# Optimization experiments

Hardware: AMD Instinct MI355X
Metric: run time of the kernel (lower is better)

Reference implementation:

```python
import jax, jax.numpy as jnp
import numpy as np

ARRAY_SIZE = 128   # crossbar rows
CBITS = 4          # psum ADC bits
LEV = 2 ** (CBITS - 1)
ALPHA = ARRAY_SIZE / LEV   # psum quant step
EPS = 1e-5

# ---- binary activation / weight quant with STE (hardtanh grad) ----
@jax.custom_vjp
def ste_sign(x):
    return jnp.where(x >= 0, 1.0, -1.0).astype(x.dtype)

def _sign_fwd(x):
    return ste_sign(x), x

def _sign_bwd(x, g):
    return (g * (jnp.abs(x) <= 1.0).astype(g.dtype),)

ste_sign.defvjp(_sign_fwd, _sign_bwd)

# ---- psum (partial-sum) quantization: cbits-level ADC over each crossbar array ----
@jax.custom_vjp
def psum_quant(p):
    return jnp.clip(jnp.round(p / ALPHA), -LEV, LEV - 1) * ALPHA

def _pq_fwd(p):
    return psum_quant(p), p

def _pq_bwd(p, g):
    return (g * (jnp.abs(p) <= ARRAY_SIZE).astype(g.dtype),)

psum_quant.defvjp(_pq_fwd, _pq_bwd)

# ---- layers ----
def bn(x, p):
    g, b, m, v = p  # each [C]
    sh = (1, -1) + (1,) * (x.ndim - 2)
    return (x - m.reshape(sh)) * (g.reshape(sh) / jnp.sqrt(v.reshape(sh) + EPS)) + b.reshape(sh)

def maxpool2(x):
    return jax.lax.reduce_window(x, -jnp.inf, jax.lax.max, (1, 1, 2, 2), (1, 1, 2, 2), 'VALID')

def conv_same(x, w):
    return jax.lax.conv_general_dilated(x, w, (1, 1), 'SAME')

def psum_conv(x, w):
    # crossbar-mapped conv: input channels split into groups of arraySize//(kh*kw),
    # each group conv'd separately, psum-quantized (ADC), then accumulated.
    O, Cin, kh, kw = w.shape
    chunk = max(1, ARRAY_SIZE // (kh * kw))
    G = -(-Cin // chunk)
    pad = G * chunk - Cin
    xp = jnp.pad(x, ((0, 0), (0, pad), (0, 0), (0, 0)))
    wp = jnp.pad(w, ((0, 0), (0, pad), (0, 0), (0, 0)))
    B, _, H, W = x.shape
    xg = xp.reshape(B, G, chunk, H, W).transpose(1, 0, 2, 3, 4)   # [G,B,c,H,W]
    wg = wp.reshape(O, G, chunk, kh, kw).transpose(1, 0, 2, 3, 4)  # [G,O,c,kh,kw]
    ps = jax.vmap(conv_same)(xg, wg)                               # [G,B,O,H,W]
    return psum_quant(ps).sum(0)

def psum_linear(x, w):
    # x [B,D], w [O,D]; D divisible by ARRAY_SIZE
    B, D = x.shape
    O = w.shape[0]
    G = D // ARRAY_SIZE
    ps = jnp.einsum('bgc,ogc->gbo', x.reshape(B, G, ARRAY_SIZE), w.reshape(O, G, ARRAY_SIZE))
    return psum_quant(ps).sum(0)


def setup_inputs() -> dict:
    key = jax.random.key(0)
    ks = iter(jax.random.split(key, 64))
    def nrm(shape, s=0.05):
        return jax.random.normal(next(ks), shape, jnp.float32) * s
    def bnp(C):
        return jnp.stack([jax.random.uniform(next(ks), (C,), jnp.float32) + 0.5,
                          nrm((C,), 0.1), nrm((C,), 0.1),
                          jax.random.uniform(next(ks), (C,), jnp.float32) + 0.5])
    return dict(
        x=jax.random.normal(next(ks), (64, 3, 32, 32), jnp.float32),
        conv0_w=nrm((128, 3, 3, 3)), bn0=bnp(128),
        w1=nrm((128, 128, 3, 3)), bn1=bnp(128),
        w2=nrm((256, 128, 3, 3)), bn2=bnp(256),
        w3=nrm((256, 256, 3, 3)), bn3=bnp(256),
        w4=nrm((512, 256, 3, 3)), bn4=bnp(512),
        w5=nrm((512, 512, 3, 3)), bn5=bnp(512),
        fc1_w=nrm((1024, 8192)), bnf1=bnp(1024),
        fc2_w=nrm((1024, 1024)), bnf2=bnp(1024),
        out_w=nrm((10, 1024)), out_b=nrm((10,)), bnout=bnp(10),
    )


def reference(x, conv0_w, bn0, w1, bn1, w2, bn2, w3, bn3, w4, bn4, w5, bn5,
              fc1_w, bnf1, fc2_w, bnf2, out_w, out_b, bnout):
    h = conv_same(x, conv0_w)                       # full-precision first conv
    h = ste_sign(bn(h, bn0))
    h = psum_conv(h, ste_sign(w1)); h = maxpool2(h); h = ste_sign(bn(h, bn1))
    h = psum_conv(h, ste_sign(w2)); h = ste_sign(bn(h, bn2))
    h = psum_conv(h, ste_sign(w3)); h = maxpool2(h); h = ste_sign(bn(h, bn3))
    h = psum_conv(h, ste_sign(w4)); h = ste_sign(bn(h, bn4))
    h = psum_conv(h, ste_sign(w5)); h = maxpool2(h); h = ste_sign(bn(h, bn5))
    h = h.reshape(h.shape[0], -1)                   # [B, 8192]
    h = ste_sign(bn(psum_linear(h, ste_sign(fc1_w)), bnf1))
    h = bn(psum_linear(h, ste_sign(fc2_w)), bnf2)   # abits=32 -> identity nonlinear
    h = h @ out_w.T + out_b
    return bn(h, bnout)
```

## Files before the change

### kernel.cpp

```cpp
#include <hip/hip_runtime.h>
#include <cstdint>
#include <cstddef>

using bf16x8 = __attribute__((ext_vector_type(8))) short;
using f32x4  = __attribute__((ext_vector_type(4))) float;
using u32x4  = __attribute__((ext_vector_type(4))) unsigned int;

#define DI __device__ __forceinline__

DI float pq16(float ps) {
    float q = rintf(ps * 0.0625f);
    q = fminf(7.f, fmaxf(-8.f, q));
    return q * 16.f;
}

DI float bnv(float x, float g, float b, float m, float v) {
    return (x - m) * (g / sqrtf(v + 1e-5f)) + b;
}

DI unsigned short sgn_bf16(float v) {
    return (v >= 0.f) ? (unsigned short)0x3F80 : (unsigned short)0xBF80;
}

__global__ __launch_bounds__(256)
void k_conv0(const float* __restrict__ x, const float* __restrict__ w,
             const float* __restrict__ bnp, unsigned short* __restrict__ out) {
    __shared__ float sX[3][3][36];
    const int b = blockIdx.x >> 5, y = blockIdx.x & 31;
    const int tid = threadIdx.x;
    const int o = tid & 127, xc = tid >> 7;

    for (int i = tid; i < 3 * 3 * 36; i += 256) {
        int col = i % 36, rr = (i / 36) % 3, c = i / 108;
        int gy = y + rr - 1, gx = col - 1;
        float v = 0.f;
        if ((unsigned)gy < 32u && (unsigned)gx < 32u)
            v = x[((b * 3 + c) * 32 + gy) * 32 + gx];
        sX[c][rr][col] = v;
    }
    float wr[27];
    const float* wp = w + o * 27;
    #pragma unroll
    for (int t = 0; t < 27; ++t) wr[t] = wp[t];
    __syncthreads();

    const float bg = bnp[o], bb = bnp[128 + o], bm = bnp[256 + o], bv = bnp[384 + o];
    unsigned short* op = out + ((size_t)(b * 32 + y) * 32) * 128 + o;

    #pragma unroll
    for (int q = 0; q < 4; ++q) {
        float acc0 = 0.f, acc1 = 0.f, acc2 = 0.f, acc3 = 0.f;
        const int X0 = xc * 16 + q * 4;
        #pragma unroll
        for (int c = 0; c < 3; ++c)
            #pragma unroll
            for (int ky = 0; ky < 3; ++ky) {
                float xv0 = sX[c][ky][X0 + 0], xv1 = sX[c][ky][X0 + 1];
                float xv2 = sX[c][ky][X0 + 2], xv3 = sX[c][ky][X0 + 3];
                float xv4 = sX[c][ky][X0 + 4], xv5 = sX[c][ky][X0 + 5];
                float w0 = wr[c * 9 + ky * 3 + 0];
                float w1 = wr[c * 9 + ky * 3 + 1];
                float w2 = wr[c * 9 + ky * 3 + 2];
                acc0 += xv0 * w0 + xv1 * w1 + xv2 * w2;
                acc1 += xv1 * w0 + xv2 * w1 + xv3 * w2;
                acc2 += xv2 * w0 + xv3 * w1 + xv4 * w2;
                acc3 += xv3 * w0 + xv4 * w1 + xv5 * w2;
            }
        op[(size_t)(X0 + 0) * 128] = sgn_bf16(bnv(acc0, bg, bb, bm, bv));
        op[(size_t)(X0 + 1) * 128] = sgn_bf16(bnv(acc1, bg, bb, bm, bv));
        op[(size_t)(X0 + 2) * 128] = sgn_bf16(bnv(acc2, bg, bb, bm, bv));
        op[(size_t)(X0 + 3) * 128] = sgn_bf16(bnv(acc3, bg, bb, bm, bv));
    }
}

__global__ __launch_bounds__(256)
void k_pack_w(const float* __restrict__ w, unsigned short* __restrict__ wpk,
              int Cin, int O, int G) {
    int idx = blockIdx.x * 256 + threadIdx.x;
    int total = G * O * 160;
    if (idx >= total) return;
    int c = idx & 15;
    int tap = (idx >> 4) % 10;
    int rest = idx / 160;
    int o = rest % O, g = rest / O;
    unsigned short v = 0;
    int cg = g * 14 + c;
    if (tap < 9 && c < 14 && cg < Cin)
        v = sgn_bf16(w[((size_t)o * Cin + cg) * 9 + tap]);
    wpk[idx] = v;
}

template <int H, int W, int Cin, int O, int G, int RH, int RW, int POOLMODE>
__global__ __launch_bounds__(256)
void k_conv_mfma(const unsigned int* __restrict__ act,
                 const unsigned short* __restrict__ wpk,
                 const float* __restrict__ bnp,
                 unsigned short* __restrict__ outa,
                 unsigned short* __restrict__ a5p) {
    constexpr int SH = RH + 2, SW = RW + 2;
    constexpr int MS = RH * RW / 16;
    constexpr int NREGX = W / RW;
    static_assert(POOLMODE != 1 || RW == 16, "pool mode 1 needs RW=16");
    static_assert(POOLMODE != 2 || (RW == 8 && MS == 4), "pool mode 2 needs 8x8");

    __shared__ __align__(16) unsigned int sA[SH * SW * 12];

    const int tid  = threadIdx.x;
    const int regY = (int)blockIdx.x / NREGX, regX = (int)blockIdx.x % NREGX;
    const int o0   = blockIdx.y * 64;
    const int b    = blockIdx.z;

    const int lane = tid & 63, wv = tid >> 6;
    const int n  = lane & 15;
    const int kb = lane >> 4;
    const int hb = kb >> 1, ch = kb & 1;

    int baseA[MS];
    #pragma unroll
    for (int ms = 0; ms < MS; ++ms) {
        int p = ms * 16 + n;
        int y = p / RW, x = p % RW;
        baseA[ms] = (y * SW + x) * 48 + ch * 16;
    }

    float tot[MS][4];
    #pragma unroll
    for (int ms = 0; ms < MS; ++ms) {
        tot[ms][0] = 0.f; tot[ms][1] = 0.f; tot[ms][2] = 0.f; tot[ms][3] = 0.f;
    }

    const unsigned short* wrow = wpk + ((size_t)o0 + wv * 16 + n) * 160 + ch * 8;

    #pragma unroll 1
    for (int g = 0; g < G; ++g) {
        const int rem_dw = (Cin - g * 14) >> 1;
        for (int i = tid; i < SH * SW * 8; i += 256) {
            int cp = i & 7, slot = i >> 3;
            int yy = slot / SW, xx = slot - yy * SW;
            int gy = regY * RH + yy - 1, gx = regX * RW + xx - 1;
            unsigned int v = 0;
            if (cp < 7 && cp < rem_dw &&
                (unsigned)gy < (unsigned)H && (unsigned)gx < (unsigned)W)
                v = act[(((size_t)b * H + gy) * W + gx) * (Cin / 2) + g * 7 + cp];
            sA[slot * 12 + cp] = v;
        }
        const unsigned short* wg = wrow + (size_t)g * O * 160;
        bf16x8 bq[5];
        #pragma unroll
        for (int s = 0; s < 5; ++s) {
            int tap = 2 * s + hb;
            bq[s] = *(const bf16x8*)(wg + tap * 16);
        }
        __syncthreads();

        const char* sAc = (const char*)sA;
        #pragma unroll
        for (int ms = 0; ms < MS; ++ms) {
            f32x4 acc = {0.f, 0.f, 0.f, 0.f};
            #pragma unroll
            for (int s = 0; s < 5; ++s) {
                const int t0 = 2 * s, t1 = 2 * s + 1;
                const int off0 = ((t0 / 3) * SW + (t0 % 3)) * 48;
                const int off1 = (t1 >= 9) ? 0 : ((t1 / 3) * SW + (t1 % 3)) * 48;
                int off = hb ? off1 : off0;
                bf16x8 af = *(const bf16x8*)(sAc + baseA[ms] + off);
                acc = __builtin_amdgcn_mfma_f32_16x16x32_bf16(af, bq[s], acc, 0, 0, 0);
            }
            tot[ms][0] += pq16(acc[0]);
            tot[ms][1] += pq16(acc[1]);
            tot[ms][2] += pq16(acc[2]);
            tot[ms][3] += pq16(acc[3]);
        }
        __syncthreads();
    }

    const int oc = o0 + wv * 16 + n;
    const float bg = bnp[oc], bb = bnp[O + oc], bm = bnp[2 * O + oc], bvr = bnp[3 * O + oc];

    if constexpr (POOLMODE == 0) {
        #pragma unroll
        for (int ms = 0; ms < MS; ++ms)
            #pragma unroll
            for (int r = 0; r < 4; ++r) {
                int p = ms * 16 + 4 * kb + r;
                int y = regY * RH + p / RW, x = regX * RW + p % RW;
                float val = bnv(tot[ms][r], bg, bb, bm, bvr);
                outa[(((size_t)b * H + y) * W + x) * O + oc] = sgn_bf16(val);
            }
    } else if constexpr (POOLMODE == 1) {
        #pragma unroll
        for (int j = 0; j < MS / 2; ++j)
            #pragma unroll
            for (int q = 0; q < 2; ++q) {
                float v = fmaxf(fmaxf(tot[2 * j][2 * q], tot[2 * j][2 * q + 1]),
                                fmaxf(tot[2 * j + 1][2 * q], tot[2 * j + 1][2 * q + 1]));
                float val = bnv(v, bg, bb, bm, bvr);
                int py = regY * (RH / 2) + j, px = regX * (RW / 2) + 2 * kb + q;
                outa[(((size_t)b * (H / 2) + py) * (W / 2) + px) * O + oc] = sgn_bf16(val);
            }
    } else {
        #pragma unroll
        for (int ms = 0; ms < MS; ++ms)
            #pragma unroll
            for (int q = 0; q < 2; ++q) {
                float h = fmaxf(tot[ms][2 * q], tot[ms][2 * q + 1]);
                float o2 = __shfl_xor(h, 32);
                float v = fmaxf(h, o2);
                if (hb == 0) {
                    float val = bnv(v, bg, bb, bm, bvr);
                    int d = oc * 16 + ms * 4 + 2 * ch + q;
                    a5p[((size_t)(d >> 3) * 64 + b) * 8 + (d & 7)] = sgn_bf16(val);
                }
            }
    }
}

template <int D, int GPB>
__global__ __launch_bounds__(256)
void k_fc_mfma(const unsigned short* __restrict__ bpk, const float* __restrict__ w,
               float* __restrict__ accg) {
    const int lane = threadIdx.x & 63, wv = threadIdx.x >> 6;
    const int n = lane & 15, kb = lane >> 4;
    const int orow = blockIdx.x * 64 + wv * 16 + n;
    const int g0 = blockIdx.y * GPB;

    float tot[4][4];
    #pragma unroll
    for (int s = 0; s < 4; ++s)
        #pragma unroll
        for (int r = 0; r < 4; ++r) tot[s][r] = 0.f;

    #pragma unroll 1
    for (int g = 0; g < GPB; ++g) {
        const int kbase = (g0 + g) * 128;
        f32x4 a0 = {0,0,0,0}, a1 = {0,0,0,0}, a2 = {0,0,0,0}, a3 = {0,0,0,0};
        #pragma unroll
        for (int s = 0; s < 4; ++s) {
            const int k0 = kbase + s * 32 + kb * 8;
            const float* wp = w + (size_t)orow * D + k0;
            float4 wlo = *(const float4*)wp;
            float4 whi = *(const float4*)(wp + 4);
            bf16x8 af;
            af[0] = (short)sgn_bf16(wlo.x); af[1] = (short)sgn_bf16(wlo.y);
            af[2] = (short)sgn_bf16(wlo.z); af[3] = (short)sgn_bf16(wlo.w);
            af[4] = (short)sgn_bf16(whi.x); af[5] = (short)sgn_bf16(whi.y);
            af[6] = (short)sgn_bf16(whi.z); af[7] = (short)sgn_bf16(whi.w);
            const unsigned short* bp = bpk + (size_t)(k0 >> 3) * 512;
            bf16x8 b0 = *(const bf16x8*)(bp + (n +  0) * 8);
            bf16x8 b1 = *(const bf16x8*)(bp + (n + 16) * 8);
            bf16x8 b2 = *(const bf16x8*)(bp + (n + 32) * 8);
            bf16x8 b3 = *(const bf16x8*)(bp + (n + 48) * 8);
            a0 = __builtin_amdgcn_mfma_f32_16x16x32_bf16(af, b0, a0, 0, 0, 0);
            a1 = __builtin_amdgcn_mfma_f32_16x16x32_bf16(af, b1, a1, 0, 0, 0);
            a2 = __builtin_amdgcn_mfma_f32_16x16x32_bf16(af, b2, a2, 0, 0, 0);
            a3 = __builtin_amdgcn_mfma_f32_16x16x32_bf16(af, b3, a3, 0, 0, 0);
        }
        #pragma unroll
        for (int r = 0; r < 4; ++r) {
            tot[0][r] += pq16(a0[r]); tot[1][r] += pq16(a1[r]);
            tot[2][r] += pq16(a2[r]); tot[3][r] += pq16(a3[r]);
        }
    }
    const int od = blockIdx.x * 64 + wv * 16 + kb * 4;
    #pragma unroll
    for (int s = 0; s < 4; ++s)
        #pragma unroll
        for (int r = 0; r < 4; ++r)
            atomicAdd(&accg[(size_t)(od + r) * 64 + s * 16 + n], tot[s][r]);
}

template <bool SIGN>
__global__ __launch_bounds__(256)
void k_fc_ep(const float* __restrict__ accg, const float* __restrict__ bnp,
             unsigned short* __restrict__ packed, float* __restrict__ h2, int O) {
    int idx = blockIdx.x * 256 + threadIdx.x;
    int b = idx & 63, o = idx >> 6;
    float val = bnv(accg[idx], bnp[o], bnp[O + o], bnp[2 * O + o], bnp[3 * O + o]);
    if (SIGN) packed[((size_t)(o >> 3) * 64 + b) * 8 + (o & 7)] = sgn_bf16(val);
    else      h2[(size_t)b * 1024 + o] = val;
}

__global__ __launch_bounds__(64)
void k_out(const float* __restrict__ h2, const float* __restrict__ ow,
           const float* __restrict__ ob, const float* __restrict__ bnp,
           float* __restrict__ out) {
    int b = blockIdx.x / 10, o = blockIdx.x % 10;
    int lane = threadIdx.x;
    float acc = 0.f;
    #pragma unroll
    for (int i = 0; i < 16; ++i) {
        int k = i * 64 + lane;
        acc += h2[b * 1024 + k] * ow[o * 1024 + k];
    }
    #pragma unroll
    for (int off = 32; off; off >>= 1) acc += __shfl_xor(acc, off);
    if (lane == 0)
        out[b * 10 + o] = bnv(acc + ob[o], bnp[o], bnp[10 + o], bnp[20 + o], bnp[30 + o]);
}

extern "C" void kernel_launch(void* const* d_in, const int* in_sizes, int n_in,
                              void* d_out, int out_size, void* d_ws, size_t ws_size,
                              hipStream_t stream) {
    const float* x     = (const float*)d_in[0];
    const float* w0    = (const float*)d_in[1];
    const float* bn0   = (const float*)d_in[2];
    const float* w1    = (const float*)d_in[3];
    const float* bn1   = (const float*)d_in[4];
    const float* w2    = (const float*)d_in[5];
    const float* bn2   = (const float*)d_in[6];
    const float* w3    = (const float*)d_in[7];
    const float* bn3   = (const float*)d_in[8];
    const float* w4    = (const float*)d_in[9];
    const float* bn4   = (const float*)d_in[10];
    const float* w5    = (const float*)d_in[11];
    const float* bn5   = (const float*)d_in[12];
    const float* fc1w  = (const float*)d_in[13];
    const float* bnf1  = (const float*)d_in[14];
    const float* fc2w  = (const float*)d_in[15];
    const float* bnf2  = (const float*)d_in[16];
    const float* outw  = (const float*)d_in[17];
    const float* outb  = (const float*)d_in[18];
    const float* bnout = (const float*)d_in[19];

    char* ws = (char*)d_ws;
    unsigned short* actA  = (unsigned short*)(ws);
    unsigned short* actB  = (unsigned short*)(ws + 16777216);
    unsigned short* wpk   = (unsigned short*)(ws + 20971520);
    unsigned short* a5p   = (unsigned short*)(ws + 27262976);
    unsigned short* a6p   = (unsigned short*)(ws + 28311552);
    float*          h1acc = (float*)(ws + 28442624);
    float*          h2acc = (float*)(ws + 28704768);
    float*          h2    = (float*)(ws + 28966912);

    const unsigned int* actA32 = (const unsigned int*)actA;
    const unsigned int* actB32 = (const unsigned int*)actB;

    hipMemsetAsync(h1acc, 0, 262144, stream);
    hipMemsetAsync(h2acc, 0, 262144, stream);

    k_conv0<<<dim3(2048), dim3(256), 0, stream>>>(x, w0, bn0, actA);

    k_pack_w<<<dim3(800), dim3(256), 0, stream>>>(w1, wpk, 128, 128, 10);
    k_conv_mfma<32, 32, 128, 128, 10, 8, 16, 1>
        <<<dim3(8, 2, 64), dim3(256), 0, stream>>>(actA32, wpk, bn1, actB, nullptr);

    k_pack_w<<<dim3(1600), dim3(256), 0, stream>>>(w2, wpk, 128, 256, 10);
    k_conv_mfma<16, 16, 128, 256, 10, 8, 16, 0>
        <<<dim3(2, 4, 64), dim3(256), 0, stream>>>(actB32, wpk, bn2, actA, nullptr);

    k_pack_w<<<dim3(3040), dim3(256), 0, stream>>>(w3, wpk, 256, 256, 19);
    k_conv_mfma<16, 16, 256, 256, 19, 8, 16, 1>
        <<<dim3(2, 4, 64), dim3(256), 0, stream>>>(actA32, wpk, bn3, actB, nullptr);

    k_pack_w<<<dim3(6080), dim3(256), 0, stream>>>(w4, wpk, 256, 512, 19);
    k_conv_mfma<8, 8, 256, 512, 19, 8, 8, 0>
        <<<dim3(1, 8, 64), dim3(256), 0, stream>>>(actB32, wpk, bn4, actA, nullptr);

    k_pack_w<<<dim3(11840), dim3(256), 0, stream>>>(w5, wpk, 512, 512, 37);
    k_conv_mfma<8, 8, 512, 512, 37, 8, 8, 2>
        <<<dim3(1, 8, 64), dim3(256), 0, stream>>>(actA32, wpk, bn5, nullptr, a5p);

    k_fc_mfma<8192, 4><<<dim3(16, 16), dim3(256), 0, stream>>>(a5p, fc1w, h1acc);
    k_fc_ep<true><<<dim3(256), dim3(256), 0, stream>>>(h1acc, bnf1, a6p, nullptr, 1024);

    k_fc_mfma<1024, 1><<<dim3(16, 8), dim3(256), 0, stream>>>(a6p, fc2w, h2acc);
    k_fc_ep<false><<<dim3(256), dim3(256), 0, stream>>>(h2acc, bnf2, nullptr, h2, 1024);

    k_out<<<dim3(640), dim3(64), 0, stream>>>(h2, outw, outb, bnout, (float*)d_out);
}
```

Before: 298.2 us.

## Prescale binary weights, precompute staging pointers, shrink conv tiles, split fc1 further

```diff
diff --git a/kernel.cpp b/kernel.cpp
--- a/kernel.cpp
+++ b/kernel.cpp
@@ -8,10 +8,11 @@
 
 #define DI __device__ __forceinline__
 
+DI float pq3(float a) {
+    return fminf(rintf(a), 7.f);
+}
 DI float pq16(float ps) {
-    float q = rintf(ps * 0.0625f);
-    q = fminf(7.f, fmaxf(-8.f, q));
-    return q * 16.f;
+    return fminf(rintf(ps * 0.0625f), 7.f) * 16.f;
 }
 
 DI float bnv(float x, float g, float b, float m, float v) {
@@ -86,7 +87,8 @@
     unsigned short v = 0;
     int cg = g * 14 + c;
     if (tap < 9 && c < 14 && cg < Cin)
-        v = sgn_bf16(w[((size_t)o * Cin + cg) * 9 + tap]);
+        v = (w[((size_t)o * Cin + cg) * 9 + tap] >= 0.f) ? (unsigned short)0x3D80
+                                                         : (unsigned short)0xBD80;
     wpk[idx] = v;
 }
 
@@ -96,10 +98,13 @@
                  const unsigned short* __restrict__ wpk,
                  const float* __restrict__ bnp,
                  unsigned short* __restrict__ outa,
-                 unsigned short* __restrict__ a5p) {
+                 unsigned short* __restrict__ a5p,
+                 const unsigned int* __restrict__ zbuf) {
     constexpr int SH = RH + 2, SW = RW + 2;
     constexpr int MS = RH * RW / 16;
     constexpr int NREGX = W / RW;
+    constexpr int SLOT8 = SH * SW * 8;
+    constexpr int NST = (SLOT8 + 255) / 256;
     static_assert(POOLMODE != 1 || RW == 16, "pool mode 1 needs RW=16");
     static_assert(POOLMODE != 2 || (RW == 8 && MS == 4), "pool mode 2 needs 8x8");
 
@@ -115,6 +120,23 @@
     const int kb = lane >> 4;
     const int hb = kb >> 1, ch = kb & 1;
 
+    const unsigned int* sptr[NST];
+    int sdst[NST];
+    #pragma unroll
+    for (int it = 0; it < NST; ++it) {
+        int i = it * 256 + tid;
+        sdst[it] = -1;
+        if (i < SLOT8) {
+            int cp = i & 7, slot = i >> 3;
+            int yy = slot / SW, xx = slot - yy * SW;
+            int gy = regY * RH + yy - 1, gx = regX * RW + xx - 1;
+            sdst[it] = slot * 12 + cp;
+            sptr[it] = ((unsigned)gy < (unsigned)H && (unsigned)gx < (unsigned)W)
+                     ? act + ((size_t)(b * H + gy) * W + gx) * (Cin / 2) + cp
+                     : zbuf + cp;
+        }
+    }
+
     int baseA[MS];
     #pragma unroll
     for (int ms = 0; ms < MS; ++ms) {
@@ -129,28 +151,23 @@
         tot[ms][0] = 0.f; tot[ms][1] = 0.f; tot[ms][2] = 0.f; tot[ms][3] = 0.f;
     }
 
-    const unsigned short* wrow = wpk + ((size_t)o0 + wv * 16 + n) * 160 + ch * 8;
+    const unsigned short* wg = wpk + ((size_t)o0 + wv * 16 + n) * 160 + ch * 8;
 
     #pragma unroll 1
     for (int g = 0; g < G; ++g) {
-        const int rem_dw = (Cin - g * 14) >> 1;
-        for (int i = tid; i < SH * SW * 8; i += 256) {
-            int cp = i & 7, slot = i >> 3;
-            int yy = slot / SW, xx = slot - yy * SW;
-            int gy = regY * RH + yy - 1, gx = regX * RW + xx - 1;
-            unsigned int v = 0;
-            if (cp < 7 && cp < rem_dw &&
-                (unsigned)gy < (unsigned)H && (unsigned)gx < (unsigned)W)
-                v = act[(((size_t)b * H + gy) * W + gx) * (Cin / 2) + g * 7 + cp];
-            sA[slot * 12 + cp] = v;
-        }
-        const unsigned short* wg = wrow + (size_t)g * O * 160;
+        #pragma unroll
+        for (int it = 0; it < NST; ++it)
+            if (sdst[it] >= 0) {
+                sA[sdst[it]] = *sptr[it];
+                sptr[it] += 7;
+            }
         bf16x8 bq[5];
         #pragma unroll
         for (int s = 0; s < 5; ++s) {
             int tap = 2 * s + hb;
             bq[s] = *(const bf16x8*)(wg + tap * 16);
         }
+        wg += O * 160;
         __syncthreads();
 
         const char* sAc = (const char*)sA;
@@ -166,10 +183,10 @@
                 bf16x8 af = *(const bf16x8*)(sAc + baseA[ms] + off);
                 acc = __builtin_amdgcn_mfma_f32_16x16x32_bf16(af, bq[s], acc, 0, 0, 0);
             }
-            tot[ms][0] += pq16(acc[0]);
-            tot[ms][1] += pq16(acc[1]);
-            tot[ms][2] += pq16(acc[2]);
-            tot[ms][3] += pq16(acc[3]);
+            tot[ms][0] += pq3(acc[0]);
+            tot[ms][1] += pq3(acc[1]);
+            tot[ms][2] += pq3(acc[2]);
+            tot[ms][3] += pq3(acc[3]);
         }
         __syncthreads();
     }
@@ -184,7 +201,7 @@
             for (int r = 0; r < 4; ++r) {
                 int p = ms * 16 + 4 * kb + r;
                 int y = regY * RH + p / RW, x = regX * RW + p % RW;
-                float val = bnv(tot[ms][r], bg, bb, bm, bvr);
+                float val = bnv(16.f * tot[ms][r], bg, bb, bm, bvr);
                 outa[(((size_t)b * H + y) * W + x) * O + oc] = sgn_bf16(val);
             }
     } else if constexpr (POOLMODE == 1) {
@@ -194,7 +211,7 @@
             for (int q = 0; q < 2; ++q) {
                 float v = fmaxf(fmaxf(tot[2 * j][2 * q], tot[2 * j][2 * q + 1]),
                                 fmaxf(tot[2 * j + 1][2 * q], tot[2 * j + 1][2 * q + 1]));
-                float val = bnv(v, bg, bb, bm, bvr);
+                float val = bnv(16.f * v, bg, bb, bm, bvr);
                 int py = regY * (RH / 2) + j, px = regX * (RW / 2) + 2 * kb + q;
                 outa[(((size_t)b * (H / 2) + py) * (W / 2) + px) * O + oc] = sgn_bf16(val);
             }
@@ -207,7 +224,7 @@
                 float o2 = __shfl_xor(h, 32);
                 float v = fmaxf(h, o2);
                 if (hb == 0) {
-                    float val = bnv(v, bg, bb, bm, bvr);
+                    float val = bnv(16.f * v, bg, bb, bm, bvr);
                     int d = oc * 16 + ms * 4 + 2 * ch + q;
                     a5p[((size_t)(d >> 3) * 64 + b) * 8 + (d & 7)] = sgn_bf16(val);
                 }
@@ -331,40 +348,40 @@
     float*          h1acc = (float*)(ws + 28442624);
     float*          h2acc = (float*)(ws + 28704768);
     float*          h2    = (float*)(ws + 28966912);
+    unsigned int*   zbuf  = (unsigned int*)(ws + 29229056);
 
     const unsigned int* actA32 = (const unsigned int*)actA;
     const unsigned int* actB32 = (const unsigned int*)actB;
 
     hipMemsetAsync(h1acc, 0, 262144, stream);
     hipMemsetAsync(h2acc, 0, 262144, stream);
+    hipMemsetAsync(zbuf, 0, 4096, stream);
 
     k_conv0<<<dim3(2048), dim3(256), 0, stream>>>(x, w0, bn0, actA);
 
     k_pack_w<<<dim3(800), dim3(256), 0, stream>>>(w1, wpk, 128, 128, 10);
-    k_conv_mfma<32, 32, 128, 128, 10, 8, 16, 1>
-        <<<dim3(8, 2, 64), dim3(256), 0, stream>>>(actA32, wpk, bn1, actB, nullptr);
+    k_conv_mfma<32, 32, 128, 128, 10, 4, 16, 1>
+        <<<dim3(16, 2, 64), dim3(256), 0, stream>>>(actA32, wpk, bn1, actB, nullptr, zbuf);
 
     k_pack_w<<<dim3(1600), dim3(256), 0, stream>>>(w2, wpk, 128, 256, 10);
-    k_conv_mfma<16, 16, 128, 256, 10, 8, 16, 0>
-        <<<dim3(2, 4, 64), dim3(256), 0, stream>>>(actB32, wpk, bn2, actA, nullptr);
+    k_conv_mfma<16, 16, 128, 256, 10, 4, 16, 0>
+        <<<dim3(4, 4, 64), dim3(256), 0, stream>>>(actB32, wpk, bn2, actA, nullptr, zbuf);
 
     k_pack_w<<<dim3(3040), dim3(256), 0, stream>>>(w3, wpk, 256, 256, 19);
-    k_conv_mfma<16, 16, 256, 256, 19, 8, 16, 1>
-        <<<dim3(2, 4, 64), dim3(256), 0, stream>>>(actA32, wpk, bn3, actB, nullptr);
+    k_conv_mfma<16, 16, 256, 256, 19, 4, 16, 1>
+        <<<dim3(4, 4, 64), dim3(256), 0, stream>>>(actA32, wpk, bn3, actB, nullptr, zbuf);
 
     k_pack_w<<<dim3(6080), dim3(256), 0, stream>>>(w4, wpk, 256, 512, 19);
     k_conv_mfma<8, 8, 256, 512, 19, 8, 8, 0>
-        <<<dim3(1, 8, 64), dim3(256), 0, stream>>>(actB32, wpk, bn4, actA, nullptr);
+        <<<dim3(1, 8, 64), dim3(256), 0, stream>>>(actB32, wpk, bn4, actA, nullptr, zbuf);
 
     k_pack_w<<<dim3(11840), dim3(256), 0, stream>>>(w5, wpk, 512, 512, 37);
     k_conv_mfma<8, 8, 512, 512, 37, 8, 8, 2>
-        <<<dim3(1, 8, 64), dim3(256), 0, stream>>>(actA32, wpk, bn5, nullptr, a5p);
-
-    k_fc_mfma<8192, 4><<<dim3(16, 16), dim3(256), 0, stream>>>(a5p, fc1w, h1acc);
+        <<<dim3(1, 8, 64), dim3(256), 0, stream>>>(actA32, wpk, bn5, nullptr, a5p, zbuf);
+
+    k_fc_mfma<8192, 1><<<dim3(16, 64), dim3(256), 0, stream>>>(a5p, fc1w, h1acc);
     k_fc_ep<true><<<dim3(256), dim3(256), 0, stream>>>(h1acc, bnf1, a6p, nullptr, 1024);
-
     k_fc_mfma<1024, 1><<<dim3(16, 8), dim3(256), 0, stream>>>(a6p, fc2w, h2acc);
     k_fc_ep<false><<<dim3(256), dim3(256), 0, stream>>>(h2acc, bnf2, nullptr, h2, 1024);
-
     k_out<<<dim3(640), dim3(64), 0, stream>>>(h2, outw, outb, bnout, (float*)d_out);
 }
```

Result: faster. 286.3 us (-4.0%).
